# Kernel optimization log

Measured on AMD Instinct MI355X. Metric: run time of the kernel, lower is better.

## Reference

```python
import jax, jax.numpy as jnp
import numpy as np

EPS = 1e-6  # F.pairwise_distance default eps, added to the difference


def setup_inputs() -> dict:
    key = jax.random.key(0)
    k1, k2 = jax.random.split(key)
    N, NS, NQ, D = 2048, 5, 8, 256
    x = jax.random.normal(k1, (N, NS + NQ, D), dtype=jnp.float32)
    label = jax.random.randint(k2, (N,), 0, N, dtype=jnp.int64)
    return {"x": x, "label": label, "n_s": NS, "n_q": NQ}


def reference(x, label, n_s, n_q):
    # x: [N, n_s+n_q, D]
    anchors = jnp.mean(x[:, :n_s, :], axis=1)               # [N, D] prototypes
    N, D = anchors.shape
    queries = x[:, n_s:n_s + n_q, :].reshape(N * n_q, D)     # [N*n_q, D]

    # Exact ||q - a + eps||^2 via GEMM expansion (matches F.pairwise_distance(.,.)**2):
    # ||q-a||^2 + 2*eps*sum(q-a) + D*eps^2
    q_sq = jnp.sum(queries * queries, axis=-1)               # [N*n_q]
    a_sq = jnp.sum(anchors * anchors, axis=-1)               # [N]
    cross = queries @ anchors.T                              # [N*n_q, N]
    q_sum = jnp.sum(queries, axis=-1)                        # [N*n_q]
    a_sum = jnp.sum(anchors, axis=-1)                        # [N]
    dist_sq = (q_sq[:, None] + a_sq[None, :] - 2.0 * cross
               + 2.0 * EPS * (q_sum[:, None] - a_sum[None, :])
               + D * EPS * EPS)
    logits = -dist_sq                                        # [N*n_q, N]

    lab = jnp.repeat(label, n_q)                             # [N*n_q]
    logp = jax.nn.log_softmax(logits, axis=-1)
    nloss = -jnp.mean(jnp.take_along_axis(logp, lab[:, None], axis=1))
    prec1 = jnp.mean((jnp.argmax(logits, axis=-1) == lab).astype(jnp.float32)) * 100.0
    return nloss, prec1
```

## Files before the change

### kernel.cpp

```cpp
#include <hip/hip_runtime.h>
#include <math.h>

#define EPS  1e-6f
#define DD   256
#define NSUP 5
#define NQ   8
#define SEQ  13
#define L2E  1.44269504088896f
#define LN2  0.693147180559945f
#define NEP  2048
#define NROW 16384
#define NCOL 2048

typedef short bf16x8 __attribute__((ext_vector_type(8)));
typedef unsigned short u16x4 __attribute__((ext_vector_type(4)));
typedef float f32x4  __attribute__((ext_vector_type(4)));

__device__ __forceinline__ ushort f2bf(float f) {
  union { float f; unsigned u; } v; v.f = f;
  unsigned r = v.u + 0x7FFFu + ((v.u >> 16) & 1u);
  return (ushort)(r >> 16);
}
__device__ __forceinline__ float bf2f(short u) {
  union { unsigned u; float f; } v; v.u = ((unsigned)(unsigned short)u) << 16;
  return v.f;
}

__global__ __launch_bounds__(256) void proto_prep(
    const float* __restrict__ x, float* __restrict__ cb,
    ushort* __restrict__ Asw, ushort* __restrict__ Qsw,
    float* __restrict__ accum, int* __restrict__ fincount) {
  const int tid = threadIdx.x, g = tid >> 6, l = tid & 63;
  const int n = blockIdx.x * 4 + g;
  if (blockIdx.x == 0 && tid == 0) { accum[0] = 0.f; accum[1] = 0.f; fincount[0] = 0; }

  const float4* xr4 = (const float4*)(x + (size_t)n * SEQ * DD);

  const int d0   = l * 4;
  const int kk   = d0 >> 5, quad = (d0 >> 3) & 3, j = d0 & 7;
  const size_t chunk_d = (size_t)kk * 64 + (size_t)quad * 16;

  float4 a = {0.f, 0.f, 0.f, 0.f};
  #pragma unroll
  for (int s = 0; s < NSUP; ++s) {
    float4 v = xr4[s * 64 + l];
    a.x += v.x; a.y += v.y; a.z += v.z; a.w += v.w;
  }
  a.x *= 0.2f; a.y *= 0.2f; a.z *= 0.2f; a.w *= 0.2f;
  {
    const size_t idx = (((size_t)(n >> 4) * 8) * 64 + chunk_d + (n & 15)) * 8 + j;
    u16x4 o = {f2bf(a.x), f2bf(a.y), f2bf(a.z), f2bf(a.w)};
    *(u16x4*)(Asw + idx) = o;
  }
  float s1 = a.x + a.y + a.z + a.w;
  float s2 = a.x * a.x + a.y * a.y + a.z * a.z + a.w * a.w;
  #pragma unroll
  for (int off = 32; off; off >>= 1) {
    s1 += __shfl_xor(s1, off);
    s2 += __shfl_xor(s2, off);
  }
  if (l == 0) cb[n] = -L2E * (s2 - 2.f * EPS * s1);

  #pragma unroll
  for (int s = 0; s < NQ; ++s) {
    float4 q = xr4[(NSUP + s) * 64 + l];
    const int row = n * NQ + s;
    const size_t idx = (((size_t)(row >> 4) * 8) * 64 + chunk_d + (row & 15)) * 8 + j;
    u16x4 o = {f2bf(q.x), f2bf(q.y), f2bf(q.z), f2bf(q.w)};
    *(u16x4*)(Qsw + idx) = o;
  }
}

__global__ __launch_bounds__(1024, 4) void proto_main(
    const ushort* __restrict__ Qsw, const ushort* __restrict__ Asw,
    const float* __restrict__ cb, const int* __restrict__ label,
    float* __restrict__ partm, float* __restrict__ parts,
    int* __restrict__ partbi, float* __restrict__ slabws) {
  const int tid  = threadIdx.x;
  const int wid  = tid >> 6, lane = tid & 63;
  const int quad = lane >> 4, lcol = lane & 15;
  const int rowg = wid & 3, colg = wid >> 2;
  const int rb   = blockIdx.x >> 1;
  const int colc = blockIdx.x & 1;
  const int r0   = rb * 128;

  const bf16x8* qb = (const bf16x8*)Qsw;
  const bf16x8* bb = (const bf16x8*)Asw;

  __shared__ bf16x8 Bl[4][2][8][64];
  __shared__ float  sCb[1024];

  sCb[tid] = cb[colc * 1024 + tid];

  bf16x8 af[2][8];
  #pragma unroll
  for (int set = 0; set < 2; ++set) {
    const size_t base = ((size_t)(rb * 8 + rowg * 2 + set) * 8) * 64 + lane;
    #pragma unroll
    for (int kk = 0; kk < 8; ++kk) af[set][kk] = qb[base + (size_t)kk * 64];
  }

  float m[2][4], s[2][4];
  int   bi[2][4];
  #pragma unroll
  for (int set = 0; set < 2; ++set)
    #pragma unroll
    for (int i = 0; i < 4; ++i) {
      m[set][i] = -1e30f; s[set][i] = 0.f; bi[set][i] = 0x7fffffff;
    }

  const int kk0 = rowg * 2;
  auto stage = [&](int tl, int b) {
    const int T = colc * 64 + colg * 16 + tl;
    #pragma unroll
    for (int k2 = 0; k2 < 2; ++k2) {
      const int kk = kk0 + k2;
      const ushort* src = Asw + (((size_t)T * 8 + kk) * 64 + lane) * 8;
      __builtin_amdgcn_global_load_lds(
          (const __attribute__((address_space(1))) void*)src,
          (__attribute__((address_space(3))) void*)&Bl[colg][b][kk][0],
          16, 0, 0);
    }
  };

  auto compute = [&](int tl, int b) {
    f32x4 c0 = {0.f, 0.f, 0.f, 0.f}, c1 = {0.f, 0.f, 0.f, 0.f};
    #pragma unroll
    for (int kk = 0; kk < 8; ++kk) {
      bf16x8 bf = Bl[colg][b][kk][lane];
      c0 = __builtin_amdgcn_mfma_f32_16x16x32_bf16(af[0][kk], bf, c0, 0, 0, 0);
      c1 = __builtin_amdgcn_mfma_f32_16x16x32_bf16(af[1][kk], bf, c1, 0, 0, 0);
    }
    const int   lcIdx  = (colg * 16 + tl) * 16 + lcol;
    const int   colIdx = colc * 1024 + lcIdx;
    const float cbv    = sCb[lcIdx];
    #pragma unroll
    for (int set = 0; set < 2; ++set) {
      #pragma unroll
      for (int i = 0; i < 4; ++i) {
        float cv = set ? c1[i] : c0[i];
        float v2 = fmaf(cv, 2.f * L2E, cbv);
        float dv = v2 - m[set][i];
        bool  gt = dv > 0.f;
        float e  = exp2f(-fabsf(dv));
        s[set][i]  = fmaf(s[set][i], gt ? e : 1.f, gt ? 1.f : e);
        m[set][i]  = fmaxf(m[set][i], v2);
        bi[set][i] = gt ? colIdx : bi[set][i];
      }
    }
  };

  stage(0, 0);
  __syncthreads();

  #pragma unroll 1
  for (int t = 0; t < 16; t += 2) {
    stage(t + 1, 1);
    compute(t, 0);
    __syncthreads();
    if (t + 2 < 16) stage(t + 2, 0);
    compute(t + 1, 1);
    __syncthreads();
  }

  #pragma unroll
  for (int mask = 1; mask < 16; mask <<= 1) {
    #pragma unroll
    for (int set = 0; set < 2; ++set)
      #pragma unroll
      for (int i = 0; i < 4; ++i) {
        float om = __shfl_xor(m[set][i], mask);
        float os = __shfl_xor(s[set][i], mask);
        int   oi = __shfl_xor(bi[set][i], mask);
        float nm = fmaxf(m[set][i], om);
        s[set][i] = s[set][i] * exp2f(m[set][i] - nm) + os * exp2f(om - nm);
        bool better = (om > m[set][i]) || (om == m[set][i] && oi < bi[set][i]);
        bi[set][i] = better ? oi : bi[set][i];
        m[set][i]  = nm;
      }
  }

  __shared__ float sm[4][128], ssh[4][128];
  __shared__ int   sbi[4][128];
  if (lcol == 0) {
    #pragma unroll
    for (int set = 0; set < 2; ++set)
      #pragma unroll
      for (int i = 0; i < 4; ++i) {
        int rl = rowg * 32 + set * 16 + quad * 4 + i;
        sm[colg][rl] = m[set][i]; ssh[colg][rl] = s[set][i]; sbi[colg][rl] = bi[set][i];
      }
  }
  __syncthreads();

  if (tid < 128) {
    float mm = sm[0][tid], sv = ssh[0][tid];
    int   b  = sbi[0][tid];
    #pragma unroll
    for (int w = 1; w < 4; ++w) {
      float om = sm[w][tid], os = ssh[w][tid];
      int   oi = sbi[w][tid];
      float nm = fmaxf(mm, om);
      sv = sv * exp2f(mm - nm) + os * exp2f(om - nm);
      bool better = (om > mm) || (om == mm && oi < b);
      b = better ? oi : b;
      mm = nm;
    }
    const int row = r0 + tid;
    partm [colc * NROW + row] = mm;
    parts [colc * NROW + row] = sv;
    partbi[colc * NROW + row] = b;
  }

  if (colc == 0) {
    const int rl = tid >> 3, l = tid & 7;
    const int row = r0 + rl;
    const int lab = label[row >> 3];
    const int kk  = l;
    float dot = 0.f;
    const size_t qc = ((size_t)(row >> 4) * 8 + kk) * 64 + (row & 15);
    const size_t ac = ((size_t)(lab >> 4) * 8 + kk) * 64 + (lab & 15);
    #pragma unroll
    for (int qd = 0; qd < 4; ++qd) {
      bf16x8 qv = qb[qc + qd * 16];
      bf16x8 av = bb[ac + qd * 16];
      #pragma unroll
      for (int j = 0; j < 8; ++j) dot = fmaf(bf2f(qv[j]), bf2f(av[j]), dot);
    }
    dot += __shfl_xor(dot, 1);
    dot += __shfl_xor(dot, 2);
    dot += __shfl_xor(dot, 4);
    if (l == 0) slabws[row] = fmaf(dot, 2.f * L2E, cb[lab]);
  }
}

__global__ __launch_bounds__(256) void proto_merge(
    const float* __restrict__ partm, const float* __restrict__ parts,
    const int* __restrict__ partbi, const float* __restrict__ slabws,
    const int* __restrict__ label,
    float* __restrict__ accum, int* __restrict__ fincount,
    float* __restrict__ out) {
  const int tid = threadIdx.x, row = blockIdx.x * 256 + tid;
  const int wid = tid >> 6;

  float m0 = partm[row],  m1 = partm[NROW + row];
  float s0 = parts[row],  s1 = parts[NROW + row];
  int   b0 = partbi[row], b1 = partbi[NROW + row];
  float nm = fmaxf(m0, m1);
  float sv = s0 * exp2f(m0 - nm) + s1 * exp2f(m1 - nm);
  bool better = (m1 > m0) || (m1 == m0 && b1 < b0);
  int  b  = better ? b1 : b0;

  const int lb = label[row >> 3];
  float loss = LN2 * (nm + log2f(sv) - slabws[row]);
  float corr = (b == lb) ? 1.f : 0.f;

  #pragma unroll
  for (int mask = 32; mask; mask >>= 1) {
    loss += __shfl_xor(loss, mask);
    corr += __shfl_xor(corr, mask);
  }
  __shared__ float red[2][4];
  if ((tid & 63) == 0) { red[0][wid] = loss; red[1][wid] = corr; }
  __syncthreads();
  if (tid == 0) {
    float L = red[0][0] + red[0][1] + red[0][2] + red[0][3];
    float C = red[1][0] + red[1][1] + red[1][2] + red[1][3];
    atomicAdd(&accum[0], L);
    atomicAdd(&accum[1], C);
    __threadfence();
    if (atomicAdd(fincount, 1) == (int)gridDim.x - 1) {
      out[0] = atomicAdd(&accum[0], 0.f) / (float)NROW;
      out[1] = atomicAdd(&accum[1], 0.f) * 100.f / (float)NROW;
    }
  }
}

extern "C" void kernel_launch(void* const* d_in, const int* in_sizes, int n_in,
                              void* d_out, int out_size, void* d_ws, size_t ws_size,
                              hipStream_t stream) {
  const float* x     = (const float*)d_in[0];
  const int*   label = (const int*)d_in[1];
  float* out = (float*)d_out;

  float*  W        = (float*)d_ws;
  float*  accum    = W;
  int*    fincount = (int*)(W + 2);
  float*  cb       = W + 16;
  ushort* Asw      = (ushort*)(cb + NCOL);
  ushort* Qsw      = Asw + (size_t)NCOL * DD;
  float*  partm    = (float*)(Qsw + (size_t)NROW * DD);
  float*  parts    = partm + 2 * NROW;
  int*    partbi   = (int*)(parts + 2 * NROW);
  float*  slabws   = (float*)(partbi + 2 * NROW);

  hipLaunchKernelGGL(proto_prep, dim3(NEP / 4), dim3(256), 0, stream,
                     x, cb, Asw, Qsw, accum, fincount);
  hipLaunchKernelGGL(proto_main, dim3(256), dim3(1024), 0, stream,
                     Qsw, Asw, cb, label, partm, parts, partbi, slabws);
  hipLaunchKernelGGL(proto_merge, dim3(NROW / 256), dim3(256), 0, stream,
                     partm, parts, partbi, slabws, label, accum, fincount, out);
}
```

Measured before the change: 119.0 us.

## Retile main kernel to 256-row blocks with 4-way column split

The main GEMM+online-softmax kernel is retiled. Each 1024-thread block now covers 256 query rows with 8 row-groups and 2 column-groups, and the anchor columns are split into 4 chunks instead of 2. Each B tile loaded into LDS is now shared by 8 row-waves instead of 4, which cuts B-tile traffic per row. The merge kernel combines 4 partials per row instead of 2, and the label-dot work is redistributed. In exchange, there are more partial results to write and merge, and less column work per block.

```diff
diff --git a/kernel.cpp b/kernel.cpp
--- a/kernel.cpp
+++ b/kernel.cpp
@@ -79,23 +79,23 @@
   const int tid  = threadIdx.x;
   const int wid  = tid >> 6, lane = tid & 63;
   const int quad = lane >> 4, lcol = lane & 15;
-  const int rowg = wid & 3, colg = wid >> 2;
-  const int rb   = blockIdx.x >> 1;
-  const int colc = blockIdx.x & 1;
-  const int r0   = rb * 128;
+  const int rowg = wid & 7, colg = wid >> 3;
+  const int rb   = blockIdx.x >> 2;
+  const int colc = blockIdx.x & 3;
+  const int r0   = rb * 256;
 
   const bf16x8* qb = (const bf16x8*)Qsw;
   const bf16x8* bb = (const bf16x8*)Asw;
 
-  __shared__ bf16x8 Bl[4][2][8][64];
-  __shared__ float  sCb[1024];
-
-  sCb[tid] = cb[colc * 1024 + tid];
+  __shared__ bf16x8 Bl[2][2][8][64];
+  __shared__ float  sCb[512];
+
+  if (tid < 512) sCb[tid] = cb[colc * 512 + tid];
 
   bf16x8 af[2][8];
   #pragma unroll
   for (int set = 0; set < 2; ++set) {
-    const size_t base = ((size_t)(rb * 8 + rowg * 2 + set) * 8) * 64 + lane;
+    const size_t base = ((size_t)(rb * 16 + rowg * 2 + set) * 8) * 64 + lane;
     #pragma unroll
     for (int kk = 0; kk < 8; ++kk) af[set][kk] = qb[base + (size_t)kk * 64];
   }
@@ -109,18 +109,13 @@
       m[set][i] = -1e30f; s[set][i] = 0.f; bi[set][i] = 0x7fffffff;
     }
 
-  const int kk0 = rowg * 2;
   auto stage = [&](int tl, int b) {
-    const int T = colc * 64 + colg * 16 + tl;
-    #pragma unroll
-    for (int k2 = 0; k2 < 2; ++k2) {
-      const int kk = kk0 + k2;
-      const ushort* src = Asw + (((size_t)T * 8 + kk) * 64 + lane) * 8;
-      __builtin_amdgcn_global_load_lds(
-          (const __attribute__((address_space(1))) void*)src,
-          (__attribute__((address_space(3))) void*)&Bl[colg][b][kk][0],
-          16, 0, 0);
-    }
+    const int T = colc * 32 + colg * 16 + tl;
+    const ushort* src = Asw + (((size_t)T * 8 + rowg) * 64 + lane) * 8;
+    __builtin_amdgcn_global_load_lds(
+        (const __attribute__((address_space(1))) void*)src,
+        (__attribute__((address_space(3))) void*)&Bl[colg][b][rowg][0],
+        16, 0, 0);
   };
 
   auto compute = [&](int tl, int b) {
@@ -132,7 +127,7 @@
       c1 = __builtin_amdgcn_mfma_f32_16x16x32_bf16(af[1][kk], bf, c1, 0, 0, 0);
     }
     const int   lcIdx  = (colg * 16 + tl) * 16 + lcol;
-    const int   colIdx = colc * 1024 + lcIdx;
+    const int   colIdx = colc * 512 + lcIdx;
     const float cbv    = sCb[lcIdx];
     #pragma unroll
     for (int set = 0; set < 2; ++set) {
@@ -180,8 +175,8 @@
       }
   }
 
-  __shared__ float sm[4][128], ssh[4][128];
-  __shared__ int   sbi[4][128];
+  __shared__ float sm[2][256], ssh[2][256];
+  __shared__ int   sbi[2][256];
   if (lcol == 0) {
     #pragma unroll
     for (int set = 0; set < 2; ++set)
@@ -193,13 +188,12 @@
   }
   __syncthreads();
 
-  if (tid < 128) {
+  if (tid < 256) {
     float mm = sm[0][tid], sv = ssh[0][tid];
     int   b  = sbi[0][tid];
-    #pragma unroll
-    for (int w = 1; w < 4; ++w) {
-      float om = sm[w][tid], os = ssh[w][tid];
-      int   oi = sbi[w][tid];
+    {
+      float om = sm[1][tid], os = ssh[1][tid];
+      int   oi = sbi[1][tid];
       float nm = fmaxf(mm, om);
       sv = sv * exp2f(mm - nm) + os * exp2f(om - nm);
       bool better = (om > mm) || (om == mm && oi < b);
@@ -213,23 +207,25 @@
   }
 
   if (colc == 0) {
-    const int rl = tid >> 3, l = tid & 7;
+    const int rl = tid >> 2, l = tid & 3;
     const int row = r0 + rl;
     const int lab = label[row >> 3];
-    const int kk  = l;
     float dot = 0.f;
-    const size_t qc = ((size_t)(row >> 4) * 8 + kk) * 64 + (row & 15);
-    const size_t ac = ((size_t)(lab >> 4) * 8 + kk) * 64 + (lab & 15);
-    #pragma unroll
-    for (int qd = 0; qd < 4; ++qd) {
-      bf16x8 qv = qb[qc + qd * 16];
-      bf16x8 av = bb[ac + qd * 16];
+    #pragma unroll
+    for (int c = 0; c < 2; ++c) {
+      const int kk = l * 2 + c;
+      const size_t qc = ((size_t)(row >> 4) * 8 + kk) * 64 + (row & 15);
+      const size_t ac = ((size_t)(lab >> 4) * 8 + kk) * 64 + (lab & 15);
       #pragma unroll
-      for (int j = 0; j < 8; ++j) dot = fmaf(bf2f(qv[j]), bf2f(av[j]), dot);
+      for (int qd = 0; qd < 4; ++qd) {
+        bf16x8 qv = qb[qc + qd * 16];
+        bf16x8 av = bb[ac + qd * 16];
+        #pragma unroll
+        for (int j = 0; j < 8; ++j) dot = fmaf(bf2f(qv[j]), bf2f(av[j]), dot);
+      }
     }
     dot += __shfl_xor(dot, 1);
     dot += __shfl_xor(dot, 2);
-    dot += __shfl_xor(dot, 4);
     if (l == 0) slabws[row] = fmaf(dot, 2.f * L2E, cb[lab]);
   }
 }
@@ -243,16 +239,21 @@
   const int tid = threadIdx.x, row = blockIdx.x * 256 + tid;
   const int wid = tid >> 6;
 
-  float m0 = partm[row],  m1 = partm[NROW + row];
-  float s0 = parts[row],  s1 = parts[NROW + row];
-  int   b0 = partbi[row], b1 = partbi[NROW + row];
-  float nm = fmaxf(m0, m1);
-  float sv = s0 * exp2f(m0 - nm) + s1 * exp2f(m1 - nm);
-  bool better = (m1 > m0) || (m1 == m0 && b1 < b0);
-  int  b  = better ? b1 : b0;
+  float mm = partm[row], sv = parts[row];
+  int   b  = partbi[row];
+  #pragma unroll
+  for (int c = 1; c < 4; ++c) {
+    float om = partm[c * NROW + row], os = parts[c * NROW + row];
+    int   oi = partbi[c * NROW + row];
+    float nm = fmaxf(mm, om);
+    sv = sv * exp2f(mm - nm) + os * exp2f(om - nm);
+    bool better = (om > mm) || (om == mm && oi < b);
+    b = better ? oi : b;
+    mm = nm;
+  }
 
   const int lb = label[row >> 3];
-  float loss = LN2 * (nm + log2f(sv) - slabws[row]);
+  float loss = LN2 * (mm + log2f(sv) - slabws[row]);
   float corr = (b == lb) ? 1.f : 0.f;
 
   #pragma unroll
@@ -290,9 +291,9 @@
   ushort* Asw      = (ushort*)(cb + NCOL);
   ushort* Qsw      = Asw + (size_t)NCOL * DD;
   float*  partm    = (float*)(Qsw + (size_t)NROW * DD);
-  float*  parts    = partm + 2 * NROW;
-  int*    partbi   = (int*)(parts + 2 * NROW);
-  float*  slabws   = (float*)(partbi + 2 * NROW);
+  float*  parts    = partm + 4 * NROW;
+  int*    partbi   = (int*)(parts + 4 * NROW);
+  float*  slabws   = (float*)(partbi + 4 * NROW);
 
   hipLaunchKernelGGL(proto_prep, dim3(NEP / 4), dim3(256), 0, stream,
                      x, cb, Asw, Qsw, accum, fincount);
```

New measurement: 125.5 us. 1.05x slower.
